# Kernel optimization log

Measured on AMD Instinct MI355X. Metric: run time of the kernel, lower is better.

Reference implementation:

```python
import jax, jax.numpy as jnp
import numpy as np
import math

V, L, H, D, T_MAX, FF = 50257, 12, 12, 768, 1024, 3072
B, T = 2, 1024
HD = D // H


def layernorm(x, g, b, eps=1e-5):
    m = x.mean(-1, keepdims=True)
    v = ((x - m) ** 2).mean(-1, keepdims=True)
    return (x - m) / jnp.sqrt(v + eps) * g + b


def mgelu(x):
    # note: module uses 0.047715 (not the standard 0.044715)
    return 0.5 * x * (1.0 + jnp.tanh(math.sqrt(2.0 / math.pi) * (x + 0.047715 * x ** 3)))


def setup_inputs() -> dict:
    key = jax.random.key(0)
    ks = jax.random.split(key, 16)
    s = 0.02
    sr = 0.02 * (2 * L) ** -0.5  # residual-projection init per GPT2 paper
    inp = {
        "idx": jax.random.randint(ks[0], (B, T), 0, V),
        "targets": jax.random.randint(ks[1], (B, T), 0, V),
        "wte": jax.random.normal(ks[2], (V, D), jnp.float32) * s,
        "wpe": jax.random.normal(ks[3], (T_MAX, D), jnp.float32) * s,
        "ln1_g": jnp.ones((L, D), jnp.float32),
        "ln1_b": jnp.zeros((L, D), jnp.float32),
        "qkv_w": jax.random.normal(ks[4], (L, D, 3 * D), jnp.float32) * s,
        "qkv_b": jnp.zeros((L, 3 * D), jnp.float32),
        "po_w": jax.random.normal(ks[5], (L, D, D), jnp.float32) * sr,
        "po_b": jnp.zeros((L, D), jnp.float32),
        "ln2_g": jnp.ones((L, D), jnp.float32),
        "ln2_b": jnp.zeros((L, D), jnp.float32),
        "fc_w": jax.random.normal(ks[6], (L, D, FF), jnp.float32) * s,
        "fc_b": jnp.zeros((L, FF), jnp.float32),
        "pr_w": jax.random.normal(ks[7], (L, FF, D), jnp.float32) * sr,
        "pr_b": jnp.zeros((L, D), jnp.float32),
        "lnf_g": jnp.ones((D,), jnp.float32),
        "lnf_b": jnp.zeros((D,), jnp.float32),
        "lm_w": jax.random.normal(ks[8], (D, V), jnp.float32) * s,
    }
    return inp


def gpt_forward(idx, targets, wte, wpe, ln1_g, ln1_b, qkv_w, qkv_b, po_w, po_b,
                ln2_g, ln2_b, fc_w, fc_b, pr_w, pr_b, lnf_g, lnf_b, lm_w):
    Bt, Tt = idx.shape
    x = wte[idx] + wpe[:Tt]  # [B,T,D]
    causal = jnp.tril(jnp.ones((Tt, Tt), bool))
    scale = 1.0 / math.sqrt(HD)

    def block(x, p):
        g1, b1, wq, bq, wo, bo, g2, b2, wf, bf, wp, bp = p
        h = layernorm(x, g1, b1)
        qkv = h @ wq + bq  # [B,T,3D]
        q, k, v = jnp.split(qkv, 3, axis=-1)
        q = q.reshape(Bt, Tt, H, HD)
        k = k.reshape(Bt, Tt, H, HD)
        v = v.reshape(Bt, Tt, H, HD)
        att = jnp.einsum('bqhd,bkhd->bhqk', q, k) * scale
        att = jnp.where(causal, att, -jnp.inf)
        att = jax.nn.softmax(att, axis=-1)  # dropout = identity (eval)
        y = jnp.einsum('bhqk,bkhd->bqhd', att, v).reshape(Bt, Tt, D)
        x = x + y @ wo + bo
        h2 = layernorm(x, g2, b2)
        x = x + mgelu(h2 @ wf + bf) @ wp + bp
        return x, None

    x, _ = jax.lax.scan(block, x, (ln1_g, ln1_b, qkv_w, qkv_b, po_w, po_b,
                                   ln2_g, ln2_b, fc_w, fc_b, pr_w, pr_b))
    x = layernorm(x, lnf_g, lnf_b)
    logits = x @ lm_w  # [B,T,V]

    logp = jax.nn.log_softmax(logits, axis=-1)
    valid = targets >= 0  # ignore_index=-1
    tgt = jnp.where(valid, targets, 0)
    nll = -jnp.take_along_axis(logp, tgt[..., None], axis=-1)[..., 0]
    loss = (nll * valid).sum() / valid.sum()
    return logits, loss


def reference(idx, targets, wte, wpe, ln1_g, ln1_b, qkv_w, qkv_b, po_w, po_b,
              ln2_g, ln2_b, fc_w, fc_b, pr_w, pr_b, lnf_g, lnf_b, lm_w):
    return gpt_forward(idx, targets, wte, wpe, ln1_g, ln1_b, qkv_w, qkv_b, po_w, po_b,
                       ln2_g, ln2_b, fc_w, fc_b, pr_w, pr_b, lnf_g, lnf_b, lm_w)
```

## Files before the change

### kernel.cpp

```cpp
#include <hip/hip_runtime.h>
#include <hip/hip_bf16.h>
#include <math.h>

#define VOC 50257
#define NL 12
#define NH 12
#define DM 768
#define FF 3072
#define BB 2
#define TT 1024
#define MR (BB*TT)

typedef __attribute__((ext_vector_type(8))) short bf16x8;
typedef __attribute__((ext_vector_type(4))) float f32x4;

__device__ __forceinline__ float mgelu_f(float x) {
    return 0.5f*x*(1.f + tanhf(0.7978845608028654f*(x + 0.047715f*x*x*x)));
}

__device__ __forceinline__ unsigned short f2bf(float f) {
    __hip_bfloat16 h = __float2bfloat16(f);
    return *reinterpret_cast<unsigned short*>(&h);
}

#define GLDS(gptr, lptr) __builtin_amdgcn_global_load_lds( \
    (const __attribute__((address_space(1))) void*)(gptr), \
    (__attribute__((address_space(3))) void*)(lptr), 16, 0, 0)

__device__ __forceinline__ int xcd_work(int bid, int total) {
    int xcd = bid & 7;
    int seq = bid >> 3;
    int q = total >> 3, r = total & 7;
    int base = (xcd < r) ? xcd*(q+1) : r + xcd*q;
    return base + seq;
}

__global__ void embed_kernel(const int* __restrict__ idx, const float* __restrict__ wte,
                             const float* __restrict__ wpe, float* __restrict__ x) {
    int row = blockIdx.x;
    int t = row % TT;
    int tok = idx[row];
    for (int d = threadIdx.x; d < DM; d += blockDim.x)
        x[(size_t)row*DM + d] = wte[(size_t)tok*DM + d] + wpe[(size_t)t*DM + d];
}

__global__ __launch_bounds__(256) void ln_kernel(const float* __restrict__ x,
                          const float* __restrict__ g,
                          const float* __restrict__ b, __hip_bfloat16* __restrict__ out) {
    int row = blockIdx.x*4 + (threadIdx.x >> 6);
    int lane = threadIdx.x & 63;
    const float* xr = x + (size_t)row*DM;
    float vals[DM/64];
    float s = 0.f;
    #pragma unroll
    for (int i = 0; i < DM/64; i++) { vals[i] = xr[lane + i*64]; s += vals[i]; }
    #pragma unroll
    for (int off = 32; off > 0; off >>= 1) s += __shfl_xor(s, off);
    float mean = s * (1.0f/DM);
    float vs = 0.f;
    #pragma unroll
    for (int i = 0; i < DM/64; i++) { float d = vals[i]-mean; vs += d*d; }
    #pragma unroll
    for (int off = 32; off > 0; off >>= 1) vs += __shfl_xor(vs, off);
    float rstd = rsqrtf(vs * (1.0f/DM) + 1e-5f);
    #pragma unroll
    for (int i = 0; i < DM/64; i++) {
        int d = lane + i*64;
        out[(size_t)row*DM + d] = __float2bfloat16((vals[i]-mean)*rstd*g[d] + b[d]);
    }
}

struct TJob { const float* in; __hip_bfloat16* out; int R, C, cx, tile0; };

__device__ __forceinline__ void trans_one(const TJob& j, int t) {
    __shared__ float tile[32][33];
    int bx = t % j.cx, by = t / j.cx;
    int c0 = bx*32, r0 = by*32;
    int tx = threadIdx.x, ty = threadIdx.y;
    #pragma unroll
    for (int i = ty; i < 32; i += 8) {
        int r = r0 + i, c = c0 + tx;
        tile[i][tx] = (r < j.R && c < j.C) ? j.in[(size_t)r*j.C + c] : 0.f;
    }
    __syncthreads();
    #pragma unroll
    for (int i = ty; i < 32; i += 8) {
        int c = c0 + i, r = r0 + tx;
        if (c < j.C && r < j.R) j.out[(size_t)c*j.R + r] = __float2bfloat16(tile[tx][i]);
    }
}

__global__ void trans4_kernel(TJob j0, TJob j1, TJob j2, TJob j3) {
    int t = blockIdx.x;
    if (t >= j3.tile0)      trans_one(j3, t - j3.tile0);
    else if (t >= j2.tile0) trans_one(j2, t - j2.tile0);
    else if (t >= j1.tile0) trans_one(j1, t - j1.tile0);
    else                    trans_one(j0, t);
}

__global__ void trans1_kernel(TJob j0) { trans_one(j0, blockIdx.x); }

template<int MODE, int HALFM>
__global__ __launch_bounds__(256) void mfma_gemm_kernel(
        const __hip_bfloat16* __restrict__ A,
        const __hip_bfloat16* __restrict__ Wt,
        const float* __restrict__ bias,
        const float* __restrict__ res,
        void* __restrict__ Cout,
        __hip_bfloat16* __restrict__ vt,
        float* __restrict__ part,
        int M, int N, int K) {
    constexpr int BM = HALFM ? 64 : 128;
    constexpr int NF = HALFM ? 2 : 4;
    constexpr int ABYTES = 2*BM*64;
    constexpr int SMEMB = (MODE == 0) ? 36864 : (ABYTES + 16384);
    __shared__ __align__(16) char smem[SMEMB];
    char* As = smem;
    char* Bs = smem + ABYTES;
    int tid = threadIdx.x;
    int lane = tid & 63, wid = tid >> 6;
    int kq = lane >> 4, lr = lane & 15;

    int nby = M / BM;
    int work = xcd_work(blockIdx.x, gridDim.x);
    int by = work % nby;
    int bx = work / nby;
    int m0 = by * BM, n0 = bx * 128;

    int wm = HALFM ? 0 : (wid >> 1);
    int wn = HALFM ? wid : (wid & 1);
    int colbase = HALFM ? wn*32 : wn*64;

    f32x4 acc[4][NF] = {};

    auto STAGE = [&](int buf, int k0) {
        if constexpr (HALFM) {
            GLDS(A + (size_t)(m0 + lane)*K + k0 + wid*8, As + buf*(BM*64) + wid*1024);
            #pragma unroll
            for (int t = 0; t < 2; t++) {
                int lx = wid + t*4;
                int r  = (lx & 1)*64 + lane;
                int kk = (lx >> 1)*8;
                int nr = n0 + r; if (nr > N-1) nr = N-1;
                GLDS(Wt + (size_t)nr*K + k0 + kk, Bs + buf*8192 + lx*1024);
            }
        } else {
            #pragma unroll
            for (int t = 0; t < 2; t++) {
                int lx = wid + t*4;
                int r  = (lx & 1)*64 + lane;
                int kk = (lx >> 1)*8;
                GLDS(A + (size_t)(m0 + r)*K + k0 + kk, As + buf*(BM*64) + lx*1024);
                int nr = n0 + r; if (nr > N-1) nr = N-1;
                GLDS(Wt + (size_t)nr*K + k0 + kk, Bs + buf*8192 + lx*1024);
            }
        }
    };

    int nk = K >> 5;
    STAGE(0, 0);
    __syncthreads();
    for (int ki = 0; ki < nk; ++ki) {
        int cur = ki & 1;
        if (ki + 1 < nk) STAGE(cur ^ 1, (ki+1)*32);

        bf16x8 afrag[4], bfrag[NF];
        #pragma unroll
        for (int m = 0; m < 4; m++)
            afrag[m] = *(const bf16x8*)(As + cur*(BM*64) + kq*(BM*16) + (wm*64 + m*16 + lr)*16);
        #pragma unroll
        for (int n = 0; n < NF; n++)
            bfrag[n] = *(const bf16x8*)(Bs + cur*8192 + kq*2048 + (colbase + n*16 + lr)*16);
        #pragma unroll
        for (int m = 0; m < 4; m++)
            #pragma unroll
            for (int n = 0; n < NF; n++)
                acc[m][n] = __builtin_amdgcn_mfma_f32_16x16x32_bf16(afrag[m], bfrag[n], acc[m][n], 0, 0, 0);
        __syncthreads();
    }

    if (MODE == 0) {
        float* eps = (float*)smem;
        int nbx = (N + 127) >> 7;
        int rl2 = tid >> 1, sub = tid & 1;
        float pm = -INFINITY, ps = 0.f;
        #pragma unroll
        for (int hh = 0; hh < 2; ++hh) {
            __syncthreads();
            if (wn == hh) {
                #pragma unroll
                for (int m = 0; m < 4; m++)
                    #pragma unroll
                    for (int n = 0; n < 4; n++) {
                        int cl = n*16 + lr;
                        #pragma unroll
                        for (int j = 0; j < 4; j++)
                            eps[(wm*64 + m*16 + kq*4 + j)*68 + cl] = acc[m][n][j];
                    }
            }
            __syncthreads();
            #pragma unroll
            for (int it = 0; it < 8; ++it) {
                int rl = it*16 + (tid >> 4);
                int c4 = tid & 15;
                int col = n0 + hh*64 + c4*4;
                int row = m0 + rl;
                f32x4 v = *(const f32x4*)(eps + rl*68 + c4*4);
                if (col + 3 < N) {
                    __builtin_nontemporal_store(v, (f32x4*)&((float*)Cout)[(size_t)row*N + col]);
                } else {
                    #pragma unroll
                    for (int u = 0; u < 4; ++u)
                        if (col + u < N)
                            __builtin_nontemporal_store(v[u], &((float*)Cout)[(size_t)row*N + col + u]);
                }
            }
            #pragma unroll
            for (int i = 0; i < 8; ++i) {
                f32x4 v = *(const f32x4*)(eps + rl2*68 + sub*32 + i*4);
                #pragma unroll
                for (int u = 0; u < 4; ++u) {
                    int col = n0 + hh*64 + sub*32 + i*4 + u;
                    float xv = (col < N) ? v[u] : -INFINITY;
                    if (xv > pm) { ps = ps*__expf(pm - xv); pm = xv; ps += 1.f; }
                    else ps += __expf(xv - pm);
                }
            }
        }
        float m2 = __shfl_xor(pm, 1), s2 = __shfl_xor(ps, 1);
        float Mx = fmaxf(pm, m2);
        float Sx = ps*__expf(pm - Mx) + s2*__expf(m2 - Mx);
        if (sub == 0)
            ((float2*)part)[(size_t)(m0 + rl2)*nbx + bx] = make_float2(Mx, Sx);
        return;
    }

    #pragma unroll
    for (int m = 0; m < 4; m++) {
        #pragma unroll
        for (int n = 0; n < NF; n++) {
            int col = n0 + colbase + n*16 + lr;
            if (col >= N) continue;
            float bv = bias[col];
            #pragma unroll
            for (int j = 0; j < 4; j++) {
                int row = m0 + wm*64 + m*16 + kq*4 + j;
                float v = acc[m][n][j] + bv;
                size_t o = (size_t)row*N + col;
                if (MODE == 1) {
                    __hip_bfloat16 bvv = __float2bfloat16(v);
                    ((__hip_bfloat16*)Cout)[o] = bvv;
                    if (col >= 2*DM) {
                        int hh = (col - 2*DM) >> 6, dd = (col - 2*DM) & 63;
                        int bb = row >> 10, tt = row & 1023;
                        vt[(((size_t)bb*NH + hh)*64 + dd)*TT + tt] = bvv;
                    }
                } else if (MODE == 2) {
                    ((float*)Cout)[o] = v + res[o];
                } else {
                    ((__hip_bfloat16*)Cout)[o] = __float2bfloat16(mgelu_f(v));
                }
            }
        }
    }
}

__global__ __launch_bounds__(256) void mfma_attn_kernel(const __hip_bfloat16* __restrict__ qkv,
                                                        const __hip_bfloat16* __restrict__ vt,
                                                        __hip_bfloat16* __restrict__ y) {
    __shared__ __align__(16) char K_lds[2][8192];
    __shared__ __align__(16) char VT_lds[2][8192];
    __shared__ __align__(16) char P_lds[4][2048];

    int work = xcd_work(blockIdx.x, BB*NH*16);
    int qt = 15 - (work & 15);
    int bh = work >> 4;
    int h  = bh % NH;
    int b  = bh / NH;
    int tid = threadIdx.x;
    int lane = tid & 63, w = tid >> 6;
    int lr = lane & 15, kq = lane >> 4;
    int q0 = qt * 64;

    int sr = lane >> 3;
    int scb = (lane & 7) * 16;

    int qrow = q0 + w*16 + lr;
    const __hip_bfloat16* qp = qkv + (size_t)(b*TT + qrow)*3*DM + h*64;
    bf16x8 qfrag[2];
    qfrag[0] = *(const bf16x8*)(qp + kq*8);
    qfrag[1] = *(const bf16x8*)(qp + 32 + kq*8);

    f32x4 oacc[4] = {};
    float m_run = -INFINITY, l_run = 0.f;
    const float scale = 0.125f;

    const char* kbase  = (const char*)qkv + ((size_t)b*TT*3*DM + DM + h*64)*2;
    const char* vtbase = (const char*)vt + ((size_t)(b*NH + h)*64)*TT*2;

    auto STAGE = [&](int buf, int kt) {
        int kv0 = kt*64;
        #pragma unroll
        for (int t = 0; t < 2; t++) {
            int lx = w + t*4;
            int r = lx*8 + sr;
            int cbs = scb ^ ((r & 7) << 4);
            GLDS(kbase + (size_t)(kv0 + r)*3*DM*2 + cbs, K_lds[buf] + lx*1024);
            GLDS(vtbase + (size_t)r*TT*2 + kv0*2 + cbs, VT_lds[buf] + lx*1024);
        }
    };

    STAGE(0, 0);
    __syncthreads();
    for (int kt = 0; kt <= qt; ++kt) {
        int cur = kt & 1;
        if (kt < qt) STAGE(cur ^ 1, kt + 1);

        f32x4 st[4] = {};
        #pragma unroll
        for (int t = 0; t < 4; ++t) {
            #pragma unroll
            for (int ks = 0; ks < 2; ++ks) {
                int row = t*16 + lr;
                bf16x8 kf = *(const bf16x8*)(K_lds[cur] + row*128 + ((ks*64 + kq*16) ^ ((lr&7)<<4)));
                st[t] = __builtin_amdgcn_mfma_f32_16x16x32_bf16(kf, qfrag[ks], st[t], 0,0,0);
            }
        }

        float sv[4][4];
        bool diag = (kt == qt);
        float pmax = -INFINITY;
        #pragma unroll
        for (int t = 0; t < 4; ++t)
            #pragma unroll
            for (int jj = 0; jj < 4; ++jj) {
                float s = st[t][jj] * scale;
                if (diag && (t*16 + kq*4 + jj > w*16 + lr)) s = -INFINITY;
                sv[t][jj] = s;
                pmax = fmaxf(pmax, s);
            }
        pmax = fmaxf(pmax, __shfl_xor(pmax, 16));
        pmax = fmaxf(pmax, __shfl_xor(pmax, 32));
        float m_new = fmaxf(m_run, pmax);
        float corr = __expf(m_run - m_new);
        float rsum = 0.f;
        #pragma unroll
        for (int t = 0; t < 4; ++t)
            #pragma unroll
            for (int jj = 0; jj < 4; ++jj) {
                float p = __expf(sv[t][jj] - m_new);
                sv[t][jj] = p;
                rsum += p;
            }
        rsum += __shfl_xor(rsum, 16);
        rsum += __shfl_xor(rsum, 32);
        l_run = l_run * corr + rsum;
        m_run = m_new;

        #pragma unroll
        for (int jj = 0; jj < 4; ++jj) {
            float c = __shfl(corr, kq*20 + jj);
            #pragma unroll
            for (int nt = 0; nt < 4; ++nt) oacc[nt][jj] *= c;
        }

        #pragma unroll
        for (int t = 0; t < 4; ++t) {
            unsigned pk0 = (unsigned)f2bf(sv[t][0]) | ((unsigned)f2bf(sv[t][1]) << 16);
            unsigned pk1 = (unsigned)f2bf(sv[t][2]) | ((unsigned)f2bf(sv[t][3]) << 16);
            unsigned off = ((unsigned)(lr*128 + t*32 + kq*8)) ^ (((unsigned)lr&7u)<<4);
            *(uint2*)(P_lds[w] + off) = make_uint2(pk0, pk1);
        }

        #pragma unroll
        for (int ks = 0; ks < 2; ++ks) {
            bf16x8 pa = *(const bf16x8*)(P_lds[w] +
                ((unsigned)(lr*128 + ((ks*64 + kq*16) ^ ((lr&7)<<4)))));
            #pragma unroll
            for (int nt = 0; nt < 4; ++nt) {
                int row = nt*16 + lr;
                bf16x8 vf = *(const bf16x8*)(VT_lds[cur] + row*128 + ((ks*64 + kq*16) ^ ((lr&7)<<4)));
                oacc[nt] = __builtin_amdgcn_mfma_f32_16x16x32_bf16(pa, vf, oacc[nt], 0,0,0);
            }
        }
        __syncthreads();
    }

    #pragma unroll
    for (int jj = 0; jj < 4; ++jj) {
        float li = __shfl(l_run, kq*20 + jj);
        int qg = q0 + w*16 + kq*4 + jj;
        #pragma unroll
        for (int nt = 0; nt < 4; ++nt)
            y[(size_t)(b*TT + qg)*DM + h*64 + nt*16 + lr] =
                __float2bfloat16(oacc[nt][jj] / li);
    }
}

__global__ void zero_acc_kernel(float* p) { p[threadIdx.x] = 0.f; }

__global__ __launch_bounds__(64) void loss_reduce_kernel(const float* __restrict__ part,
                                                         const float* __restrict__ logits,
                                                         const int* __restrict__ targets,
                                                         float* __restrict__ acc) {
    int row = blockIdx.x;
    int lane = threadIdx.x;
    const int nbx = (VOC + 127) >> 7;
    float m = -INFINITY, s = 0.f;
    for (int bx = lane; bx < nbx; bx += 64) {
        float2 p = ((const float2*)part)[(size_t)row*nbx + bx];
        float Mx = fmaxf(m, p.x);
        s = s*__expf(m - Mx) + p.y*__expf(p.x - Mx);
        m = Mx;
    }
    #pragma unroll
    for (int off = 32; off > 0; off >>= 1) {
        float m2 = __shfl_xor(m, off), s2 = __shfl_xor(s, off);
        float Mx = fmaxf(m, m2);
        s = s*__expf(m - Mx) + s2*__expf(m2 - Mx);
        m = Mx;
    }
    if (lane == 0) {
        int tgt = targets[row];
        if (tgt >= 0) {
            float lse = logf(s) + m;
            atomicAdd(&acc[0], lse - logits[(size_t)row*VOC + tgt]);
            atomicAdd(&acc[1], 1.f);
        }
    }
}

__global__ void loss_final_kernel(const float* acc, float* out) {
    out[0] = acc[0] / acc[1];
}

static inline TJob mkjob(const float* in, __hip_bfloat16* out, int R, int C, int tile0) {
    TJob j; j.in = in; j.out = out; j.R = R; j.C = C;
    j.cx = (C + 31)/32; j.tile0 = tile0;
    return j;
}

extern "C" void kernel_launch(void* const* d_in, const int* in_sizes, int n_in,
                              void* d_out, int out_size, void* d_ws, size_t ws_size,
                              hipStream_t stream) {
    const int*   idx     = (const int*)  d_in[0];
    const int*   targets = (const int*)  d_in[1];
    const float* wte     = (const float*)d_in[2];
    const float* wpe     = (const float*)d_in[3];
    const float* ln1_g   = (const float*)d_in[4];
    const float* ln1_b   = (const float*)d_in[5];
    const float* qkv_w   = (const float*)d_in[6];
    const float* qkv_b   = (const float*)d_in[7];
    const float* po_w    = (const float*)d_in[8];
    const float* po_b    = (const float*)d_in[9];
    const float* ln2_g   = (const float*)d_in[10];
    const float* ln2_b   = (const float*)d_in[11];
    const float* fc_w    = (const float*)d_in[12];
    const float* fc_b    = (const float*)d_in[13];
    const float* pr_w    = (const float*)d_in[14];
    const float* pr_b    = (const float*)d_in[15];
    const float* lnf_g   = (const float*)d_in[16];
    const float* lnf_b   = (const float*)d_in[17];
    const float* lm_w    = (const float*)d_in[18];

    float* logits = (float*)d_out;

    char* p = (char*)d_ws;
    float* x = (float*)p;                 p += (size_t)MR*DM*4;
    __hip_bfloat16* h    = (__hip_bfloat16*)p; p += (size_t)MR*DM*2;
    __hip_bfloat16* qkvb = (__hip_bfloat16*)p; p += (size_t)MR*3*DM*2;
    __hip_bfloat16* yb   = (__hip_bfloat16*)p; p += (size_t)MR*DM*2;
    __hip_bfloat16* fb   = (__hip_bfloat16*)p; p += (size_t)MR*FF*2;
    __hip_bfloat16* vtb  = (__hip_bfloat16*)p; p += (size_t)BB*NH*64*TT*2;
    __hip_bfloat16* lm_wt  = (__hip_bfloat16*)p; p += (size_t)VOC*DM*2;
    __hip_bfloat16* qkv_wt = (__hip_bfloat16*)p; p += (size_t)3*DM*DM*2;
    __hip_bfloat16* po_wt  = (__hip_bfloat16*)p; p += (size_t)DM*DM*2;
    __hip_bfloat16* fc_wt  = (__hip_bfloat16*)p; p += (size_t)FF*DM*2;
    __hip_bfloat16* pr_wt  = (__hip_bfloat16*)p; p += (size_t)DM*FF*2;
    float* part = (float*)p;              p += (size_t)MR*((VOC+127)/128)*2*4;
    float* lacc = (float*)p;

    dim3 tpb(32, 8);

    embed_kernel<<<MR, 256, 0, stream>>>(idx, wte, wpe, x);

    {
        TJob j = mkjob(lm_w, lm_wt, DM, VOC, 0);
        int tiles = j.cx * ((DM+31)/32);
        trans1_kernel<<<tiles, tpb, 0, stream>>>(j);
    }

    for (int l = 0; l < NL; l++) {
        TJob j0 = mkjob(qkv_w + (size_t)l*DM*3*DM, qkv_wt, DM, 3*DM, 0);
        int t1 = j0.cx * 24;
        TJob j1 = mkjob(po_w + (size_t)l*DM*DM, po_wt, DM, DM, t1);
        int t2 = t1 + j1.cx * 24;
        TJob j2 = mkjob(fc_w + (size_t)l*DM*FF, fc_wt, DM, FF, t2);
        int t3 = t2 + j2.cx * 24;
        TJob j3 = mkjob(pr_w + (size_t)l*FF*DM, pr_wt, FF, DM, t3);
        int tot = t3 + j3.cx * 96;
        trans4_kernel<<<tot, tpb, 0, stream>>>(j0, j1, j2, j3);

        ln_kernel<<<MR/4, 256, 0, stream>>>(x, ln1_g + l*DM, ln1_b + l*DM, h);
        mfma_gemm_kernel<1,0><<<(3*DM/128)*(MR/128), 256, 0, stream>>>(
            h, qkv_wt, qkv_b + (size_t)l*3*DM, nullptr, qkvb, vtb, nullptr, MR, 3*DM, DM);
        mfma_attn_kernel<<<BB*NH*(TT/64), 256, 0, stream>>>(qkvb, vtb, yb);
        mfma_gemm_kernel<2,1><<<(DM/128)*(MR/64), 256, 0, stream>>>(
            yb, po_wt, po_b + (size_t)l*DM, x, x, nullptr, nullptr, MR, DM, DM);
        ln_kernel<<<MR/4, 256, 0, stream>>>(x, ln2_g + l*DM, ln2_b + l*DM, h);
        mfma_gemm_kernel<3,0><<<(FF/128)*(MR/128), 256, 0, stream>>>(
            h, fc_wt, fc_b + (size_t)l*FF, nullptr, fb, nullptr, nullptr, MR, FF, DM);
        mfma_gemm_kernel<2,1><<<(DM/128)*(MR/64), 256, 0, stream>>>(
            fb, pr_wt, pr_b + (size_t)l*DM, x, x, nullptr, nullptr, MR, DM, FF);
    }

    ln_kernel<<<MR/4, 256, 0, stream>>>(x, lnf_g, lnf_b, h);
    mfma_gemm_kernel<0,0><<<((VOC+127)/128)*(MR/128), 256, 0, stream>>>(
        h, lm_wt, nullptr, nullptr, logits, nullptr, part, MR, VOC, DM);

    zero_acc_kernel<<<1, 2, 0, stream>>>(lacc);
    loss_reduce_kernel<<<MR, 64, 0, stream>>>(part, logits, targets, lacc);
    loss_final_kernel<<<1, 1, 0, stream>>>(lacc, logits + (size_t)MR*VOC);
}
```

Before: 3.107 ms.

## Triple-buffer LDS staging in GEMM and attention with explicit vmcnt waits

Result: faster. 2.868 ms (-7.7%).

```diff
diff --git a/kernel.cpp b/kernel.cpp
--- a/kernel.cpp
+++ b/kernel.cpp
@@ -112,11 +112,11 @@
         int M, int N, int K) {
     constexpr int BM = HALFM ? 64 : 128;
     constexpr int NF = HALFM ? 2 : 4;
-    constexpr int ABYTES = 2*BM*64;
-    constexpr int SMEMB = (MODE == 0) ? 36864 : (ABYTES + 16384);
+    constexpr int ABM = BM*64;
+    constexpr int SMEMB = 3*ABM + 3*8192;
     __shared__ __align__(16) char smem[SMEMB];
     char* As = smem;
-    char* Bs = smem + ABYTES;
+    char* Bs = smem + 3*ABM;
     int tid = threadIdx.x;
     int lane = tid & 63, wid = tid >> 6;
     int kq = lane >> 4, lr = lane & 15;
@@ -133,16 +133,16 @@
 
     f32x4 acc[4][NF] = {};
 
-    auto STAGE = [&](int buf, int k0) {
+    auto STAGE = [&](int slot, int k0) {
         if constexpr (HALFM) {
-            GLDS(A + (size_t)(m0 + lane)*K + k0 + wid*8, As + buf*(BM*64) + wid*1024);
+            GLDS(A + (size_t)(m0 + lane)*K + k0 + wid*8, As + slot*ABM + wid*1024);
             #pragma unroll
             for (int t = 0; t < 2; t++) {
                 int lx = wid + t*4;
                 int r  = (lx & 1)*64 + lane;
                 int kk = (lx >> 1)*8;
                 int nr = n0 + r; if (nr > N-1) nr = N-1;
-                GLDS(Wt + (size_t)nr*K + k0 + kk, Bs + buf*8192 + lx*1024);
+                GLDS(Wt + (size_t)nr*K + k0 + kk, Bs + slot*8192 + lx*1024);
             }
         } else {
             #pragma unroll
@@ -150,24 +150,30 @@
                 int lx = wid + t*4;
                 int r  = (lx & 1)*64 + lane;
                 int kk = (lx >> 1)*8;
-                GLDS(A + (size_t)(m0 + r)*K + k0 + kk, As + buf*(BM*64) + lx*1024);
+                GLDS(A + (size_t)(m0 + r)*K + k0 + kk, As + slot*ABM + lx*1024);
                 int nr = n0 + r; if (nr > N-1) nr = N-1;
-                GLDS(Wt + (size_t)nr*K + k0 + kk, Bs + buf*8192 + lx*1024);
+                GLDS(Wt + (size_t)nr*K + k0 + kk, Bs + slot*8192 + lx*1024);
             }
         }
     };
 
     int nk = K >> 5;
     STAGE(0, 0);
-    __syncthreads();
+    STAGE(1, (1 < nk ? 1 : nk-1)*32);
     for (int ki = 0; ki < nk; ++ki) {
-        int cur = ki & 1;
-        if (ki + 1 < nk) STAGE(cur ^ 1, (ki+1)*32);
+        int cur = ki % 3;
+        int k2 = (ki+2 < nk ? ki+2 : nk-1)*32;
+        STAGE((ki+2) % 3, k2);
+        __builtin_amdgcn_sched_barrier(0);
+        if constexpr (HALFM) asm volatile("s_waitcnt vmcnt(6)" ::: "memory");
+        else                 asm volatile("s_waitcnt vmcnt(8)" ::: "memory");
+        __builtin_amdgcn_s_barrier();
+        __builtin_amdgcn_sched_barrier(0);
 
         bf16x8 afrag[4], bfrag[NF];
         #pragma unroll
         for (int m = 0; m < 4; m++)
-            afrag[m] = *(const bf16x8*)(As + cur*(BM*64) + kq*(BM*16) + (wm*64 + m*16 + lr)*16);
+            afrag[m] = *(const bf16x8*)(As + cur*ABM + kq*(BM*16) + (wm*64 + m*16 + lr)*16);
         #pragma unroll
         for (int n = 0; n < NF; n++)
             bfrag[n] = *(const bf16x8*)(Bs + cur*8192 + kq*2048 + (colbase + n*16 + lr)*16);
@@ -176,7 +182,10 @@
             #pragma unroll
             for (int n = 0; n < NF; n++)
                 acc[m][n] = __builtin_amdgcn_mfma_f32_16x16x32_bf16(afrag[m], bfrag[n], acc[m][n], 0, 0, 0);
-        __syncthreads();
+
+        __builtin_amdgcn_sched_barrier(0);
+        asm volatile("s_waitcnt lgkmcnt(0)" ::: "memory");
+        __builtin_amdgcn_s_barrier();
     }
 
     if (MODE == 0) {
@@ -268,8 +277,8 @@
 __global__ __launch_bounds__(256) void mfma_attn_kernel(const __hip_bfloat16* __restrict__ qkv,
                                                         const __hip_bfloat16* __restrict__ vt,
                                                         __hip_bfloat16* __restrict__ y) {
-    __shared__ __align__(16) char K_lds[2][8192];
-    __shared__ __align__(16) char VT_lds[2][8192];
+    __shared__ __align__(16) char K_lds[3][8192];
+    __shared__ __align__(16) char VT_lds[3][8192];
     __shared__ __align__(16) char P_lds[4][2048];
 
     int work = xcd_work(blockIdx.x, BB*NH*16);
@@ -298,23 +307,27 @@
     const char* kbase  = (const char*)qkv + ((size_t)b*TT*3*DM + DM + h*64)*2;
     const char* vtbase = (const char*)vt + ((size_t)(b*NH + h)*64)*TT*2;
 
-    auto STAGE = [&](int buf, int kt) {
+    auto STAGE = [&](int slot, int kt) {
         int kv0 = kt*64;
         #pragma unroll
         for (int t = 0; t < 2; t++) {
             int lx = w + t*4;
             int r = lx*8 + sr;
             int cbs = scb ^ ((r & 7) << 4);
-            GLDS(kbase + (size_t)(kv0 + r)*3*DM*2 + cbs, K_lds[buf] + lx*1024);
-            GLDS(vtbase + (size_t)r*TT*2 + kv0*2 + cbs, VT_lds[buf] + lx*1024);
+            GLDS(kbase + (size_t)(kv0 + r)*3*DM*2 + cbs, K_lds[slot] + lx*1024);
+            GLDS(vtbase + (size_t)r*TT*2 + kv0*2 + cbs, VT_lds[slot] + lx*1024);
         }
     };
 
     STAGE(0, 0);
-    __syncthreads();
+    STAGE(1, 1 <= qt ? 1 : qt);
     for (int kt = 0; kt <= qt; ++kt) {
-        int cur = kt & 1;
-        if (kt < qt) STAGE(cur ^ 1, kt + 1);
+        int cur = kt % 3;
+        STAGE((kt+2) % 3, kt+2 <= qt ? kt+2 : qt);
+        __builtin_amdgcn_sched_barrier(0);
+        asm volatile("s_waitcnt vmcnt(8)" ::: "memory");
+        __builtin_amdgcn_s_barrier();
+        __builtin_amdgcn_sched_barrier(0);
 
         f32x4 st[4] = {};
         #pragma unroll
@@ -383,7 +396,10 @@
                 oacc[nt] = __builtin_amdgcn_mfma_f32_16x16x32_bf16(pa, vf, oacc[nt], 0,0,0);
             }
         }
-        __syncthreads();
+
+        __builtin_amdgcn_sched_barrier(0);
+        asm volatile("s_waitcnt lgkmcnt(0)" ::: "memory");
+        __builtin_amdgcn_s_barrier();
     }
 
     #pragma unroll
```
